# Kernel tuning notes

Hardware: AMD Instinct MI355X
Metric: run time of the kernel (lower is better)

## Reference

```python
import jax, jax.numpy as jnp
import numpy as np

N_FFT = 1024
HOP = 256
WIN = 1024
LENGTH = 600  # hard-coded in the module's forward


def setup_inputs() -> dict:
    key = jax.random.key(0)
    x = jax.random.normal(key, (64, 1, 513, 1024, 2), dtype=jnp.float32)
    return {"x": x}


def reference(x):
    B, C, F, T, D = x.shape
    # real/imag pair -> complex spectrogram (B, F, T)
    xc = (x[..., 0] + 1j * x[..., 1]).reshape(B, F, T)
    # onesided inverse FFT per frame (torch.fft.irfft includes 1/n scaling)
    frames = jnp.fft.irfft(xc, n=N_FFT, axis=1)  # (B, n_fft, T)
    # torch.istft default window (window arg is NOT forwarded by the wrapper):
    # ones(win_length) centered-padded to n_fft
    pad = (N_FFT - WIN) // 2
    window = jnp.pad(jnp.ones((WIN,), jnp.float32), (pad, N_FFT - WIN - pad))
    frames = frames * window[None, :, None]
    # overlap-add via scatter-add
    L = N_FFT + HOP * (T - 1)
    idx = (jnp.arange(T)[:, None] * HOP + jnp.arange(N_FFT)[None, :]).reshape(-1)
    vals = frames.transpose(0, 2, 1).reshape(B, -1)  # (B, T*n_fft)
    y = jnp.zeros((B, L), frames.dtype).at[:, idx].add(vals)
    # window-envelope normalization (sum of squared windows)
    env = jnp.zeros((L,), jnp.float32).at[idx].add(jnp.tile(window ** 2, T))
    # center=True trims n_fft//2; length=600 truncates
    start = N_FFT // 2
    y = y[:, start:start + LENGTH] / env[start:start + LENGTH]
    return y.reshape(B, C, LENGTH)
```

## Files before the change

kernel.cpp:

```cpp
#include <hip/hip_runtime.h>
#include <math.h>


#define NFREQ 513
#define NFFT  1024
#define HOP   256
#define LEN   600
#define START 512
#define NB    64
#define NT    5
#define NSEG  11

__constant__ int seg_t[NSEG]  = {0, 0,   1,   1,   1,   2, 2,   2,   3, 3,   4};
__constant__ int seg_n0[NSEG] = {512, 768, 256, 512, 768, 0, 256, 512, 0, 256, 0};
__constant__ int seg_n1[NSEG] = {768, 1024, 512, 768, 856, 256, 512, 600, 256, 344, 88};

__global__ __launch_bounds__(256) void idft_frames(const float* __restrict__ x,
                                                   float* __restrict__ S) {
    const int b   = blockIdx.x / NSEG;
    const int seg = blockIdx.x % NSEG;
    const int t   = seg_t[seg];

    __shared__ float2 X[NFREQ];

    for (int f = threadIdx.x; f < NFREQ; f += blockDim.x) {
        const float* p = x + ((long)(b * NFREQ + f) * NFFT + t) * 2;
        X[f] = make_float2(p[0], p[1]);
    }
    __syncthreads();

    const int n = seg_n0[seg] + (int)threadIdx.x;
    if (n >= seg_n1[seg]) return;

    const float w = 6.28318530717958647692f / (float)NFFT;

    float cn, sn;
    sincosf((float)n * w, &sn, &cn);

    float acc = 0.0f;

    int k = 1;
    #pragma unroll
    for (int blk = 0; blk < 4; ++blk) {
        const int kend = min(512, k + 128);
        const int m = (k * n) & (NFFT - 1);
        float c, s;
        sincosf((float)m * w, &s, &c);
        #pragma unroll 4
        for (; k < kend; ++k) {
            const float2 xv = X[k];
            acc = fmaf(xv.x, c, acc);
            acc = fmaf(-xv.y, s, acc);
            const float c2 = fmaf(c, cn, -(s * sn));
            s              = fmaf(s, cn,   c * sn);
            c = c2;
        }
    }

    const float nyq = (n & 1) ? -X[512].x : X[512].x;
    const float res = X[0].x + nyq + 2.0f * acc;

    S[((long)(b * NT + t)) * NFFT + n] = res;
}

__global__ __launch_bounds__(256) void ola_norm(const float* __restrict__ S,
                                                float* __restrict__ out) {
    const int i = blockIdx.x * blockDim.x + threadIdx.x;
    if (i >= NB * LEN) return;
    const int b  = i / LEN;
    const int lp = i - b * LEN;
    const int l  = lp + START;
    const int tlo = max(0, (l - (NFFT - HOP)) >> 8);
    const int thi = l >> 8;
    float sum = 0.0f;
    #pragma unroll
    for (int t = 0; t < NT; ++t) {
        if (t >= tlo && t <= thi) {
            sum += S[((long)(b * NT + t)) * NFFT + (l - HOP * t)];
        }
    }
    const float env = (float)(thi - tlo + 1);
    out[i] = sum / (1024.0f * env);
}

extern "C" void kernel_launch(void* const* d_in, const int* in_sizes, int n_in,
                              void* d_out, int out_size, void* d_ws, size_t ws_size,
                              hipStream_t stream) {
    const float* x = (const float*)d_in[0];
    float* out = (float*)d_out;
    float* S = (float*)d_ws;

    idft_frames<<<dim3(NB * NSEG), dim3(256), 0, stream>>>(x, S);

    const int nout = NB * LEN;
    ola_norm<<<dim3((nout + 255) / 256), dim3(256), 0, stream>>>(S, out);
}
```

Before: 312.9 us.

## Split IDFT frequency range across blocks and exploit conjugate symmetry pairing

Each output sample's frequency sum is split across two blocks. Within each block, bins k and 512-k are paired so that one twiddle recurrence serves both. The twiddle update switches to a two-term Chebyshev recurrence, and ola_norm sums the two partial results. The aim is to cut per-thread serial work and raise block-level parallelism, at the cost of each block still loading the full strided spectrum column, which doubles the gather traffic.

New measurement: 311.8 us. About the same (-0.3%).

```diff
diff --git a/kernel.cpp b/kernel.cpp
--- a/kernel.cpp
+++ b/kernel.cpp
@@ -10,6 +10,7 @@
 #define NB    64
 #define NT    5
 #define NSEG  11
+#define NSPLIT 2
 
 __constant__ int seg_t[NSEG]  = {0, 0,   1,   1,   1,   2, 2,   2,   3, 3,   4};
 __constant__ int seg_n0[NSEG] = {512, 768, 256, 512, 768, 0, 256, 512, 0, 256, 0};
@@ -17,8 +18,10 @@
 
 __global__ __launch_bounds__(256) void idft_frames(const float* __restrict__ x,
                                                    float* __restrict__ S) {
-    const int b   = blockIdx.x / NSEG;
-    const int seg = blockIdx.x % NSEG;
+    const int b   = blockIdx.x / (NSEG * NSPLIT);
+    const int r   = blockIdx.x % (NSEG * NSPLIT);
+    const int seg = r / NSPLIT;
+    const int sp  = r % NSPLIT;
     const int t   = seg_t[seg];
 
     __shared__ float2 X[NFREQ];
@@ -36,31 +39,53 @@
 
     float cn, sn;
     sincosf((float)n * w, &sn, &cn);
+    const float t2 = 2.0f * cn;
 
-    float acc = 0.0f;
+    float acc1 = 0.0f;
+    float acc2 = 0.0f;
 
-    int k = 1;
+    int k            = (sp == 0) ? 1   : 129;
+    const int ksplit = (sp == 0) ? 129 : 256;
+
     #pragma unroll
-    for (int blk = 0; blk < 4; ++blk) {
-        const int kend = min(512, k + 128);
-        const int m = (k * n) & (NFFT - 1);
-        float c, s;
-        sincosf((float)m * w, &s, &c);
-        #pragma unroll 4
-        for (; k < kend; ++k) {
-            const float2 xv = X[k];
-            acc = fmaf(xv.x, c, acc);
-            acc = fmaf(-xv.y, s, acc);
-            const float c2 = fmaf(c, cn, -(s * sn));
-            s              = fmaf(s, cn,   c * sn);
-            c = c2;
+    for (int blk = 0; blk < 2; ++blk) {
+        const int m1 = (k * n) & (NFFT - 1);
+        const int m0 = ((k - 1) * n) & (NFFT - 1);
+        float c, s, cm1, sm1;
+        sincosf((float)m1 * w, &s, &c);
+        sincosf((float)m0 * w, &sm1, &cm1);
+        const int kstop = min(ksplit, k + 64);
+        #pragma unroll 8
+        for (; k < kstop; ++k) {
+            const float2 xa = X[k];
+            const float2 xb = X[512 - k];
+            acc1 = fmaf(xa.x, c, acc1);
+            acc1 = fmaf(-xa.y, s, acc1);
+            acc2 = fmaf(xb.x, c, acc2);
+            acc2 = fmaf(xb.y, s, acc2);
+            const float cnx = fmaf(t2, c, -cm1);
+            const float snx = fmaf(t2, s, -sm1);
+            cm1 = c; sm1 = s; c = cnx; s = snx;
         }
     }
 
-    const float nyq = (n & 1) ? -X[512].x : X[512].x;
-    const float res = X[0].x + nyq + 2.0f * acc;
+    const float sigma = (n & 1) ? -1.0f : 1.0f;
+    float res = 2.0f * (acc1 + sigma * acc2);
 
-    S[((long)(b * NT + t)) * NFFT + n] = res;
+    if (sp == 0) {
+        float c256, s256;
+        switch (n & 3) {
+            case 0:  c256 = 1.0f;  s256 = 0.0f;  break;
+            case 1:  c256 = 0.0f;  s256 = 1.0f;  break;
+            case 2:  c256 = -1.0f; s256 = 0.0f;  break;
+            default: c256 = 0.0f;  s256 = -1.0f; break;
+        }
+        const float term256 = X[256].x * c256 - X[256].y * s256;
+        const float nyq = (n & 1) ? -X[512].x : X[512].x;
+        res += X[0].x + nyq + 2.0f * term256;
+    }
+
+    S[(((long)(b * NT + t)) * NSPLIT + sp) * NFFT + n] = res;
 }
 
 __global__ __launch_bounds__(256) void ola_norm(const float* __restrict__ S,
@@ -76,7 +101,8 @@
     #pragma unroll
     for (int t = 0; t < NT; ++t) {
         if (t >= tlo && t <= thi) {
-            sum += S[((long)(b * NT + t)) * NFFT + (l - HOP * t)];
+            const long base = (((long)(b * NT + t)) * NSPLIT) * NFFT + (l - HOP * t);
+            sum += S[base] + S[base + NFFT];
         }
     }
     const float env = (float)(thi - tlo + 1);
@@ -90,7 +116,7 @@
     float* out = (float*)d_out;
     float* S = (float*)d_ws;
 
-    idft_frames<<<dim3(NB * NSEG), dim3(256), 0, stream>>>(x, S);
+    idft_frames<<<dim3(NB * NSEG * NSPLIT), dim3(256), 0, stream>>>(x, S);
 
     const int nout = NB * LEN;
     ola_norm<<<dim3((nout + 255) / 256), dim3(256), 0, stream>>>(S, out);
```
